# Kernel optimization log

Hardware: AMD Instinct MI355X
Metric: run time of the kernel (lower is better)

Reference implementation:

```python
import jax, jax.numpy as jnp
import numpy as np

N_PROTS = 2048
MOLS_PER_PROT = 8
N_MOLS = N_PROTS * MOLS_PER_PROT
DIM = 768
MARGIN = 0.5


def setup_inputs() -> dict:
    key = jax.random.key(0)
    k1, k2, k3 = jax.random.split(key, 3)
    prot_emb = jax.random.normal(k1, (N_PROTS, DIM), dtype=jnp.float32)
    mol_emb = jax.random.normal(k2, (N_MOLS, DIM), dtype=jnp.float32)
    # L2-normalize like typical CLIP-style retrieval embeddings
    prot_emb = prot_emb / jnp.linalg.norm(prot_emb, axis=1, keepdims=True)
    mol_emb = mol_emb / jnp.linalg.norm(mol_emb, axis=1, keepdims=True)
    # block-structured labels: protein i paired with mols [8i, 8i+8)
    rows = jnp.repeat(jnp.arange(N_PROTS), MOLS_PER_PROT)
    cols = jnp.arange(N_MOLS)
    labels = jnp.zeros((N_PROTS, N_MOLS), dtype=jnp.float32).at[rows, cols].set(1.0)
    # pIC50 values in [2, 10]
    pic50_matrix = 2.0 + 8.0 * jax.random.uniform(k3, (N_PROTS, N_MOLS), dtype=jnp.float32)
    logit_scale = jnp.float32(1.0 / 0.07)
    return {"prot_emb": prot_emb, "mol_emb": mol_emb, "labels": labels,
            "pic50_matrix": pic50_matrix, "logit_scale": logit_scale}


def reference(prot_emb, mol_emb, labels, pic50_matrix, logit_scale):
    n_prots = prot_emb.shape[0]
    n_mols = mol_emb.shape[0]
    sim = jnp.matmul(prot_emb, mol_emb.T) * logit_scale  # [n_prots, n_mols]

    # affinity-weighted InfoNCE (prot -> mol)
    pic50_norm = jnp.clip((pic50_matrix - 2.0) / 8.0, 0.0, 1.0)
    pos_w = labels * pic50_norm
    pos_w = pos_w / (pos_w.sum(axis=1, keepdims=True) + 1e-8)
    loss_p2m = -jnp.sum(pos_w * jax.nn.log_softmax(sim, axis=1)) / n_prots

    # mol -> prot NLL
    mol_labels = jnp.argmax(labels, axis=0)  # [n_mols]
    lsm_m2p = jax.nn.log_softmax(sim.T, axis=1)  # [n_mols, n_prots]
    loss_m2p = -jnp.mean(lsm_m2p[jnp.arange(n_mols), mol_labels])

    # pairwise margin-ranking among positives (exactly MOLS_PER_PROT positives per protein)
    P = MOLS_PER_PROT
    _, pos_idx = jax.lax.top_k(labels, P)  # [n_prots, P] indices of positives
    pos_pic = jnp.take_along_axis(pic50_matrix, pos_idx, axis=1)  # [n_prots, P]
    pos_sc = jnp.take_along_axis(sim, pos_idx, axis=1)            # [n_prots, P]
    dp = pos_pic[:, :, None] - pos_pic[:, None, :]  # [n_prots, P, P]
    ds = pos_sc[:, :, None] - pos_sc[:, None, :]
    pair = jnp.where(dp > 0, jax.nn.relu(MARGIN - ds),
                     jnp.where(dp < 0, jax.nn.relu(MARGIN + ds), 0.0))
    upper = jnp.triu(jnp.ones((P, P), dtype=bool), k=1)  # unordered pairs j<k
    n_pairs = n_prots * (P * (P - 1) // 2)
    ranking_loss = jnp.sum(jnp.where(upper[None], pair, 0.0)) / n_pairs

    # negative push-down
    neg_loss = jnp.mean(jax.nn.relu(sim * (1.0 - labels)))

    total = loss_p2m + loss_m2p + 0.5 * ranking_loss + 0.1 * neg_loss
    return (total, loss_p2m, loss_m2p, ranking_loss, neg_loss)
```

## Files before the change

### kernel.cpp

```cpp
#include <hip/hip_runtime.h>
#include <hip/hip_bf16.h>
#include <math.h>

#define N_PROTS 2048
#define N_MOLS  16384
#define DIM     768
#define SHIFT   16.0f
#define MARGIN  0.5f

typedef __attribute__((ext_vector_type(8))) short short8;
typedef __attribute__((ext_vector_type(4))) float f32x4;
typedef __attribute__((ext_vector_type(4))) unsigned short us4;
typedef __attribute__((ext_vector_type(8))) unsigned short us8;

__device__ __forceinline__ unsigned short bf16rnd(float x) {
    unsigned int u = __float_as_uint(x);
    u += 0x7fffu + ((u >> 16) & 1u);
    return (unsigned short)(u >> 16);
}

__device__ __forceinline__ void gload16(const void* g, void* l) {
    __builtin_amdgcn_global_load_lds(
        (const __attribute__((address_space(1))) unsigned int*)g,
        (__attribute__((address_space(3))) unsigned int*)l, 16, 0, 0);
}

#define ACC_FLOATS 34824
#define PROT_BF_OFF_B 139296ull
#define PROT_BF_BYTES (2048ull*768*2)
#define MOL_BF_OFF_B  (PROT_BF_OFF_B + PROT_BF_BYTES)
#define MOL_BF_BYTES  (16384ull*768*2)
#define WS_NEED       (MOL_BF_OFF_B + MOL_BF_BYTES)

__global__ __launch_bounds__(256)
void convert_bf16(const float* __restrict__ prot, const float* __restrict__ mol,
                  unsigned short* __restrict__ protBf, unsigned short* __restrict__ molBf)
{
    const size_t PROT_G = (size_t)N_PROTS * DIM / 8;
    size_t t = (size_t)blockIdx.x * 256 + threadIdx.x;
    const float* src;
    unsigned short* dst;
    if (t < PROT_G) { src = prot + t * 8; dst = protBf + t * 8; }
    else            { size_t u = t - PROT_G; src = mol + u * 8; dst = molBf + u * 8; }
    float4 v0 = ((const float4*)src)[0];
    float4 v1 = ((const float4*)src)[1];
    us8 o;
    o[0] = bf16rnd(v0.x); o[1] = bf16rnd(v0.y); o[2] = bf16rnd(v0.z); o[3] = bf16rnd(v0.w);
    o[4] = bf16rnd(v1.x); o[5] = bf16rnd(v1.y); o[6] = bf16rnd(v1.z); o[7] = bf16rnd(v1.w);
    *(us8*)dst = o;
}

__global__ __launch_bounds__(256, 3)
void sim_pass_bf16(const unsigned short* __restrict__ protBf,
                   const unsigned short* __restrict__ molBf,
                   const float* __restrict__ scale_p,
                   float* __restrict__ row_se, float* __restrict__ col_se,
                   float* __restrict__ pos_sim, float* __restrict__ scalars)
{
    __shared__ unsigned short As[128][64];
    __shared__ unsigned short Bs[128][64];
    __shared__ float redBuf[4];

    const int tid = threadIdx.x;
    const int l    = blockIdx.x;
    const int xcd  = l & 7;
    const int slot = l >> 3;
    const int bx   = xcd * 16 + (slot & 15);
    const int by   = slot >> 4;
    const int rowBase = by * 128;
    const int colBase = bx * 128;

    const int wave = tid >> 6;
    const int lane = tid & 63;
    const int wr = (wave >> 1) * 64;
    const int wc = (wave & 1) * 64;
    const int l15 = lane & 15;
    const int q   = lane >> 4;

    f32x4 acc[4][4];
#pragma unroll
    for (int i = 0; i < 4; ++i)
#pragma unroll
        for (int j = 0; j < 4; ++j) acc[i][j] = (f32x4){0.f, 0.f, 0.f, 0.f};

    const int rsub = lane >> 3;
    const int cs   = lane & 7;
    const int csrc = (cs ^ rsub) << 3;
    const unsigned short* aP =
        protBf + (size_t)(rowBase + wave * 32 + rsub) * DIM + csrc;
    const unsigned short* bP =
        molBf  + (size_t)(colBase + wave * 32 + rsub) * DIM + csrc;
    unsigned short* ldsA = &As[0][0] + (wave * 32) * 64;
    unsigned short* ldsB = &Bs[0][0] + (wave * 32) * 64;

#pragma unroll 1
    for (int s = 0; s < DIM / 64; ++s) {
        __syncthreads();
#pragma unroll
        for (int i = 0; i < 4; ++i) {
            gload16(aP + (size_t)i * 8 * DIM + s * 64, ldsA + i * 8 * 64);
            gload16(bP + (size_t)i * 8 * DIM + s * 64, ldsB + i * 8 * 64);
        }
        __syncthreads();

#pragma unroll
        for (int kk = 0; kk < 2; ++kk) {
            short8 aF[4], bF[4];
#pragma unroll
            for (int mi = 0; mi < 4; ++mi) {
                const int R = wr + mi * 16 + l15;
                aF[mi] = *(const short8*)&As[R][((kk * 4 + q) ^ (l15 & 7)) << 3];
            }
#pragma unroll
            for (int ni = 0; ni < 4; ++ni) {
                const int R = wc + ni * 16 + l15;
                bF[ni] = *(const short8*)&Bs[R][((kk * 4 + q) ^ (l15 & 7)) << 3];
            }
#pragma unroll
            for (int mi = 0; mi < 4; ++mi)
#pragma unroll
                for (int ni = 0; ni < 4; ++ni)
                    acc[mi][ni] = __builtin_amdgcn_mfma_f32_16x16x32_bf16(
                        aF[mi], bF[ni], acc[mi][ni], 0, 0, 0);
        }
    }

    const float scale = scale_p[0];
    float rsum[4][4];
    float csum[4] = {0.f, 0.f, 0.f, 0.f};
    float rl = 0.f;
#pragma unroll
    for (int mi = 0; mi < 4; ++mi)
#pragma unroll
        for (int r = 0; r < 4; ++r) rsum[mi][r] = 0.f;

#pragma unroll
    for (int mi = 0; mi < 4; ++mi) {
#pragma unroll
        for (int ni = 0; ni < 4; ++ni) {
#pragma unroll
            for (int r = 0; r < 4; ++r) {
                float sim = acc[mi][ni][r] * scale;
                float e = __expf(sim - SHIFT);
                rsum[mi][r] += e;
                csum[ni] += e;
                rl += fmaxf(sim, 0.f);
                int rg = rowBase + wr + mi * 16 + q * 4 + r;
                int cg = colBase + wc + ni * 16 + l15;
                if ((cg >> 3) == rg) pos_sim[cg] = sim;
            }
        }
    }

#pragma unroll
    for (int mi = 0; mi < 4; ++mi) {
#pragma unroll
        for (int r = 0; r < 4; ++r) {
            float v = rsum[mi][r];
            v += __shfl_xor(v, 1); v += __shfl_xor(v, 2);
            v += __shfl_xor(v, 4); v += __shfl_xor(v, 8);
            if (l15 == 0)
                atomicAdd(&row_se[rowBase + wr + mi * 16 + q * 4 + r], v);
        }
    }
#pragma unroll
    for (int ni = 0; ni < 4; ++ni) {
        float v = csum[ni];
        v += __shfl_xor(v, 16); v += __shfl_xor(v, 32);
        if (q == 0)
            atomicAdd(&col_se[colBase + wc + ni * 16 + l15], v);
    }
#pragma unroll
    for (int m = 1; m < 64; m <<= 1) rl += __shfl_xor(rl, m);
    if (lane == 0) redBuf[wave] = rl;
    __syncthreads();
    if (tid == 0)
        atomicAdd(&scalars[0], redBuf[0] + redBuf[1] + redBuf[2] + redBuf[3]);
}

__global__ __launch_bounds__(256, 2)
void sim_pass(const float* __restrict__ prot, const float* __restrict__ mol,
              const float* __restrict__ scale_p,
              float* __restrict__ row_se, float* __restrict__ col_se,
              float* __restrict__ pos_sim, float* __restrict__ scalars)
{
    __shared__ unsigned short As[128][32];
    __shared__ unsigned short Bs[128][32];
    __shared__ float redBuf[4];

    const int tid = threadIdx.x;
    const int rowBase = blockIdx.y * 128;
    const int colBase = blockIdx.x * 128;
    const int wave = tid >> 6;
    const int lane = tid & 63;
    const int wr = (wave >> 1) * 64;
    const int wc = (wave & 1) * 64;
    const int l15 = lane & 15;
    const int q   = lane >> 4;

    f32x4 acc[4][4];
#pragma unroll
    for (int i = 0; i < 4; ++i)
#pragma unroll
        for (int j = 0; j < 4; ++j) acc[i][j] = (f32x4){0.f, 0.f, 0.f, 0.f};

    const float* aBase = prot + (size_t)rowBase * DIM;
    const float* bBase = mol  + (size_t)colBase * DIM;
    float4 aReg[4], bReg[4];
#pragma unroll
    for (int i = 0; i < 4; ++i) {
        int f = tid + 256 * i;
        int row = f >> 3, c4 = f & 7;
        aReg[i] = *(const float4*)(aBase + (size_t)row * DIM + (c4 << 2));
        bReg[i] = *(const float4*)(bBase + (size_t)row * DIM + (c4 << 2));
    }
#pragma unroll 1
    for (int s = 0; s < DIM / 32; ++s) {
#pragma unroll
        for (int i = 0; i < 4; ++i) {
            int f = tid + 256 * i;
            int row = f >> 3, c4 = f & 7;
            us4 av, bv;
            av.x = bf16rnd(aReg[i].x); av.y = bf16rnd(aReg[i].y);
            av.z = bf16rnd(aReg[i].z); av.w = bf16rnd(aReg[i].w);
            bv.x = bf16rnd(bReg[i].x); bv.y = bf16rnd(bReg[i].y);
            bv.z = bf16rnd(bReg[i].z); bv.w = bf16rnd(bReg[i].w);
            *(us4*)&As[row][c4 << 2] = av;
            *(us4*)&Bs[row][c4 << 2] = bv;
        }
        __syncthreads();
        if (s + 1 < DIM / 32) {
            int k0 = (s + 1) * 32;
#pragma unroll
            for (int i = 0; i < 4; ++i) {
                int f = tid + 256 * i;
                int row = f >> 3, c4 = f & 7;
                aReg[i] = *(const float4*)(aBase + (size_t)row * DIM + k0 + (c4 << 2));
                bReg[i] = *(const float4*)(bBase + (size_t)row * DIM + k0 + (c4 << 2));
            }
        }
        short8 aF[4], bF[4];
#pragma unroll
        for (int mi = 0; mi < 4; ++mi) aF[mi] = *(const short8*)&As[wr + mi * 16 + l15][q * 8];
#pragma unroll
        for (int ni = 0; ni < 4; ++ni) bF[ni] = *(const short8*)&Bs[wc + ni * 16 + l15][q * 8];
#pragma unroll
        for (int mi = 0; mi < 4; ++mi)
#pragma unroll
            for (int ni = 0; ni < 4; ++ni)
                acc[mi][ni] = __builtin_amdgcn_mfma_f32_16x16x32_bf16(aF[mi], bF[ni], acc[mi][ni], 0, 0, 0);
        __syncthreads();
    }

    const float scale = scale_p[0];
    float rsum[4][4];
    float csum[4] = {0.f, 0.f, 0.f, 0.f};
    float rl = 0.f;
#pragma unroll
    for (int mi = 0; mi < 4; ++mi)
#pragma unroll
        for (int r = 0; r < 4; ++r) rsum[mi][r] = 0.f;
#pragma unroll
    for (int mi = 0; mi < 4; ++mi) {
#pragma unroll
        for (int ni = 0; ni < 4; ++ni) {
#pragma unroll
            for (int r = 0; r < 4; ++r) {
                float sim = acc[mi][ni][r] * scale;
                float e = __expf(sim - SHIFT);
                rsum[mi][r] += e;
                csum[ni] += e;
                rl += fmaxf(sim, 0.f);
                int rg = rowBase + wr + mi * 16 + q * 4 + r;
                int cg = colBase + wc + ni * 16 + l15;
                if ((cg >> 3) == rg) pos_sim[cg] = sim;
            }
        }
    }
#pragma unroll
    for (int mi = 0; mi < 4; ++mi) {
#pragma unroll
        for (int r = 0; r < 4; ++r) {
            float v = rsum[mi][r];
            v += __shfl_xor(v, 1); v += __shfl_xor(v, 2);
            v += __shfl_xor(v, 4); v += __shfl_xor(v, 8);
            if (l15 == 0)
                atomicAdd(&row_se[rowBase + wr + mi * 16 + q * 4 + r], v);
        }
    }
#pragma unroll
    for (int ni = 0; ni < 4; ++ni) {
        float v = csum[ni];
        v += __shfl_xor(v, 16); v += __shfl_xor(v, 32);
        if (q == 0)
            atomicAdd(&col_se[colBase + wc + ni * 16 + l15], v);
    }
#pragma unroll
    for (int m = 1; m < 64; m <<= 1) rl += __shfl_xor(rl, m);
    if (lane == 0) redBuf[wave] = rl;
    __syncthreads();
    if (tid == 0)
        atomicAdd(&scalars[0], redBuf[0] + redBuf[1] + redBuf[2] + redBuf[3]);
}

__global__ __launch_bounds__(256)
void finalize1(const float* __restrict__ row_se, const float* __restrict__ col_se,
               const float* __restrict__ pos_sim, const float* __restrict__ pic50,
               float* __restrict__ scalars)
{
    int j = blockIdx.x * 256 + threadIdx.x;
    float m2p = SHIFT + __logf(col_se[j]) - pos_sim[j];

    float p2m = 0.f, rank = 0.f, prelu = 0.f;
    if ((j & 7) == 0) {
        int i = j >> 3;
        float s[8], pc[8], pr[8];
#pragma unroll
        for (int p = 0; p < 8; ++p) {
            s[p]  = pos_sim[j + p];
            pr[p] = pic50[(size_t)i * N_MOLS + j + p];
            float x = (pr[p] - 2.0f) * 0.125f;
            pc[p] = fminf(fmaxf(x, 0.f), 1.f);
            prelu += fmaxf(s[p], 0.f);
        }
        float wsum = 1e-8f;
#pragma unroll
        for (int p = 0; p < 8; ++p) wsum += pc[p];
        float lse = SHIFT + __logf(row_se[i]);
        float accp = 0.f;
#pragma unroll
        for (int p = 0; p < 8; ++p) accp += pc[p] * (lse - s[p]);
        p2m = accp / wsum;
#pragma unroll
        for (int a = 0; a < 8; ++a)
#pragma unroll
            for (int b = a + 1; b < 8; ++b) {
                float dp = pr[a] - pr[b];
                float ds = s[a] - s[b];
                float v = (dp > 0.f) ? fmaxf(MARGIN - ds, 0.f)
                        : ((dp < 0.f) ? fmaxf(MARGIN + ds, 0.f) : 0.f);
                rank += v;
            }
    }

#pragma unroll
    for (int m = 1; m < 64; m <<= 1) {
        m2p   += __shfl_xor(m2p, m);
        p2m   += __shfl_xor(p2m, m);
        rank  += __shfl_xor(rank, m);
        prelu += __shfl_xor(prelu, m);
    }
    __shared__ float rbuf[4][4];
    int wave = threadIdx.x >> 6, lane = threadIdx.x & 63;
    if (lane == 0) { rbuf[wave][0] = m2p; rbuf[wave][1] = p2m; rbuf[wave][2] = rank; rbuf[wave][3] = prelu; }
    __syncthreads();
    if (threadIdx.x == 0) {
        float a = 0, b = 0, c = 0, d = 0;
        for (int w = 0; w < 4; ++w) { a += rbuf[w][0]; b += rbuf[w][1]; c += rbuf[w][2]; d += rbuf[w][3]; }
        atomicAdd(&scalars[2], a);
        atomicAdd(&scalars[1], b);
        atomicAdd(&scalars[3], c);
        atomicAdd(&scalars[4], d);
    }
}

__global__ void finalize2(const float* __restrict__ scalars, float* __restrict__ out)
{
    float relu_neg = scalars[0] - scalars[4];
    float p2m  = scalars[1] / (float)N_PROTS;
    float m2p  = scalars[2] / (float)N_MOLS;
    float rank = scalars[3] / ((float)N_PROTS * 28.0f);
    float neg  = relu_neg / ((float)N_PROTS * (float)N_MOLS);
    out[0] = p2m + m2p + 0.5f * rank + 0.1f * neg;
    out[1] = p2m;
    out[2] = m2p;
    out[3] = rank;
    out[4] = neg;
}

extern "C" void kernel_launch(void* const* d_in, const int* in_sizes, int n_in,
                              void* d_out, int out_size, void* d_ws, size_t ws_size,
                              hipStream_t stream) {
    const float* prot   = (const float*)d_in[0];
    const float* mol    = (const float*)d_in[1];
    const float* pic50  = (const float*)d_in[3];
    const float* lscale = (const float*)d_in[4];

    float* ws      = (float*)d_ws;
    float* row_se  = ws;
    float* col_se  = ws + 2048;
    float* pos_sim = ws + 2048 + 16384;
    float* scalars = ws + 2048 + 16384 + 16384;

    hipMemsetAsync(d_ws, 0, (size_t)ACC_FLOATS * sizeof(float), stream);

    if (ws_size >= WS_NEED) {
        unsigned short* protBf = (unsigned short*)((char*)d_ws + PROT_BF_OFF_B);
        unsigned short* molBf  = (unsigned short*)((char*)d_ws + MOL_BF_OFF_B);
        size_t groups = ((size_t)N_PROTS + N_MOLS) * DIM / 8;
        convert_bf16<<<(unsigned)(groups / 256), 256, 0, stream>>>(prot, mol, protBf, molBf);
        sim_pass_bf16<<<2048, 256, 0, stream>>>(protBf, molBf, lscale, row_se, col_se, pos_sim, scalars);
    } else {
        dim3 grid(N_MOLS / 128, N_PROTS / 128);
        sim_pass<<<grid, 256, 0, stream>>>(prot, mol, lscale, row_se, col_se, pos_sim, scalars);
    }
    finalize1<<<N_MOLS / 256, 256, 0, stream>>>(row_se, col_se, pos_sim, pic50, scalars);
    finalize2<<<1, 1, 0, stream>>>(scalars, (float*)d_out);
}
```

Before: 386.3 us.

## Use 256x256 tiles with 4-stage async LDS pipeline in bf16 sim kernel

Replaces the 128x128, 256-thread bf16 GEMM tile with a 256x256 tile on 512 threads (8 waves, each computing 128x64). Global-to-LDS loads go through a 4-slot ring buffer with three tiles prefetched ahead, a vmcnt wait plus a single barrier per k-step, and prefetches interleaved between MFMA groups under raised wave priority. The aim is more reuse per loaded byte and loads that overlap the MFMA work instead of being serialized behind two barriers. The cost is more registers (128 accumulators per lane), fewer blocks (512), and a ring that relies on a hand-tuned vmcnt count, plus dummy reloads in the tail that refetch already-used k-tiles.

```diff
diff --git a/kernel.cpp b/kernel.cpp
--- a/kernel.cpp
+++ b/kernel.cpp
@@ -50,117 +50,132 @@
     *(us8*)dst = o;
 }
 
-__global__ __launch_bounds__(256, 3)
-void sim_pass_bf16(const unsigned short* __restrict__ protBf,
-                   const unsigned short* __restrict__ molBf,
-                   const float* __restrict__ scale_p,
-                   float* __restrict__ row_se, float* __restrict__ col_se,
-                   float* __restrict__ pos_sim, float* __restrict__ scalars)
+__global__ __launch_bounds__(512, 2)
+void sim_pass_bf16_v2(const unsigned short* __restrict__ protBf,
+                      const unsigned short* __restrict__ molBf,
+                      const float* __restrict__ scale_p,
+                      float* __restrict__ row_se, float* __restrict__ col_se,
+                      float* __restrict__ pos_sim, float* __restrict__ scalars)
 {
-    __shared__ unsigned short As[128][64];
-    __shared__ unsigned short Bs[128][64];
-    __shared__ float redBuf[4];
+    __shared__ unsigned short As[4][256][32];
+    __shared__ unsigned short Bs[4][256][32];
+    __shared__ float redBuf[8];
 
     const int tid = threadIdx.x;
-    const int l    = blockIdx.x;
-    const int xcd  = l & 7;
-    const int slot = l >> 3;
-    const int bx   = xcd * 16 + (slot & 15);
-    const int by   = slot >> 4;
-    const int rowBase = by * 128;
-    const int colBase = bx * 128;
+    const int bid  = blockIdx.x;
+    const int xcd  = bid & 7;
+    const int sl8  = bid >> 3;
+    const int bx   = xcd * 8 + (sl8 & 7);
+    const int by   = sl8 >> 3;
+    const int rowBase = by * 256;
+    const int colBase = bx * 256;
 
     const int wave = tid >> 6;
     const int lane = tid & 63;
-    const int wr = (wave >> 1) * 64;
-    const int wc = (wave & 1) * 64;
+    const int wm = wave >> 2;
+    const int wn = wave & 3;
     const int l15 = lane & 15;
     const int q   = lane >> 4;
 
-    f32x4 acc[4][4];
-#pragma unroll
-    for (int i = 0; i < 4; ++i)
+    const int rsub = lane >> 2;
+    const int cs   = lane & 3;
+    const int swz  = (cs ^ (rsub & 3)) << 3;
+    const unsigned short* aP =
+        protBf + (size_t)(rowBase + wave * 32 + rsub) * DIM + swz;
+    const unsigned short* bP =
+        molBf  + (size_t)(colBase + wave * 32 + rsub) * DIM + swz;
+
+#define STAGE_A(sl, kt) do { \
+    gload16(aP + (size_t)(kt) * 32,                    &As[sl][wave * 32][0]);      \
+    gload16(aP + (size_t)(kt) * 32 + (size_t)16 * DIM, &As[sl][wave * 32 + 16][0]); \
+} while (0)
+#define STAGE_B(sl, kt) do { \
+    gload16(bP + (size_t)(kt) * 32,                    &Bs[sl][wave * 32][0]);      \
+    gload16(bP + (size_t)(kt) * 32 + (size_t)16 * DIM, &Bs[sl][wave * 32 + 16][0]); \
+} while (0)
+
+    f32x4 acc[8][4];
+#pragma unroll
+    for (int i = 0; i < 8; ++i)
 #pragma unroll
         for (int j = 0; j < 4; ++j) acc[i][j] = (f32x4){0.f, 0.f, 0.f, 0.f};
 
-    const int rsub = lane >> 3;
-    const int cs   = lane & 7;
-    const int csrc = (cs ^ rsub) << 3;
-    const unsigned short* aP =
-        protBf + (size_t)(rowBase + wave * 32 + rsub) * DIM + csrc;
-    const unsigned short* bP =
-        molBf  + (size_t)(colBase + wave * 32 + rsub) * DIM + csrc;
-    unsigned short* ldsA = &As[0][0] + (wave * 32) * 64;
-    unsigned short* ldsB = &Bs[0][0] + (wave * 32) * 64;
+    STAGE_A(0, 0); STAGE_B(0, 0);
+    STAGE_A(1, 1); STAGE_B(1, 1);
+    STAGE_A(2, 2); STAGE_B(2, 2);
+
+    const int fArow = wm * 128 + l15;
+    const int fBrow = wn * 64 + l15;
+    const int fsw   = (q ^ (l15 & 3)) << 3;
 
 #pragma unroll 1
-    for (int s = 0; s < DIM / 64; ++s) {
-        __syncthreads();
-#pragma unroll
-        for (int i = 0; i < 4; ++i) {
-            gload16(aP + (size_t)i * 8 * DIM + s * 64, ldsA + i * 8 * 64);
-            gload16(bP + (size_t)i * 8 * DIM + s * 64, ldsB + i * 8 * 64);
-        }
-        __syncthreads();
-
-#pragma unroll
-        for (int kk = 0; kk < 2; ++kk) {
-            short8 aF[4], bF[4];
-#pragma unroll
-            for (int mi = 0; mi < 4; ++mi) {
-                const int R = wr + mi * 16 + l15;
-                aF[mi] = *(const short8*)&As[R][((kk * 4 + q) ^ (l15 & 7)) << 3];
-            }
-#pragma unroll
-            for (int ni = 0; ni < 4; ++ni) {
-                const int R = wc + ni * 16 + l15;
-                bF[ni] = *(const short8*)&Bs[R][((kk * 4 + q) ^ (l15 & 7)) << 3];
-            }
-#pragma unroll
-            for (int mi = 0; mi < 4; ++mi)
-#pragma unroll
-                for (int ni = 0; ni < 4; ++ni)
-                    acc[mi][ni] = __builtin_amdgcn_mfma_f32_16x16x32_bf16(
-                        aF[mi], bF[ni], acc[mi][ni], 0, 0, 0);
-        }
-    }
+    for (int t = 0; t < 24; ++t) {
+        const int sl   = t & 3;
+        const int pf   = (t + 3) & 3;
+        const int kpre = (t < 21) ? (t + 3) : (t - 5);
+        asm volatile("s_waitcnt vmcnt(8)" ::: "memory");
+        __builtin_amdgcn_s_barrier();
+
+        short8 aF[4], bF[4];
+#pragma unroll
+        for (int ni = 0; ni < 4; ++ni)
+            bF[ni] = *(const short8*)&Bs[sl][fBrow + ni * 16][fsw];
+#pragma unroll
+        for (int mi = 0; mi < 4; ++mi)
+            aF[mi] = *(const short8*)&As[sl][fArow + mi * 16][fsw];
+        STAGE_A(pf, kpre);
+        __builtin_amdgcn_s_setprio(1);
+#pragma unroll
+        for (int mi = 0; mi < 4; ++mi)
+#pragma unroll
+            for (int ni = 0; ni < 4; ++ni)
+                acc[mi][ni] = __builtin_amdgcn_mfma_f32_16x16x32_bf16(
+                    aF[mi], bF[ni], acc[mi][ni], 0, 0, 0);
+        __builtin_amdgcn_s_setprio(0);
+
+#pragma unroll
+        for (int mi = 0; mi < 4; ++mi)
+            aF[mi] = *(const short8*)&As[sl][fArow + 64 + mi * 16][fsw];
+        STAGE_B(pf, kpre);
+        __builtin_amdgcn_s_setprio(1);
+#pragma unroll
+        for (int mi = 0; mi < 4; ++mi)
+#pragma unroll
+            for (int ni = 0; ni < 4; ++ni)
+                acc[4 + mi][ni] = __builtin_amdgcn_mfma_f32_16x16x32_bf16(
+                    aF[mi], bF[ni], acc[4 + mi][ni], 0, 0, 0);
+        __builtin_amdgcn_s_setprio(0);
+    }
+#undef STAGE_A
+#undef STAGE_B
 
     const float scale = scale_p[0];
-    float rsum[4][4];
     float csum[4] = {0.f, 0.f, 0.f, 0.f};
     float rl = 0.f;
 #pragma unroll
-    for (int mi = 0; mi < 4; ++mi)
-#pragma unroll
-        for (int r = 0; r < 4; ++r) rsum[mi][r] = 0.f;
-
-#pragma unroll
-    for (int mi = 0; mi < 4; ++mi) {
+    for (int mi = 0; mi < 8; ++mi) {
+        float rs[4] = {0.f, 0.f, 0.f, 0.f};
 #pragma unroll
         for (int ni = 0; ni < 4; ++ni) {
 #pragma unroll
             for (int r = 0; r < 4; ++r) {
                 float sim = acc[mi][ni][r] * scale;
                 float e = __expf(sim - SHIFT);
-                rsum[mi][r] += e;
+                rs[r] += e;
                 csum[ni] += e;
                 rl += fmaxf(sim, 0.f);
-                int rg = rowBase + wr + mi * 16 + q * 4 + r;
-                int cg = colBase + wc + ni * 16 + l15;
+                int rg = rowBase + wm * 128 + mi * 16 + q * 4 + r;
+                int cg = colBase + wn * 64 + ni * 16 + l15;
                 if ((cg >> 3) == rg) pos_sim[cg] = sim;
             }
         }
-    }
-
-#pragma unroll
-    for (int mi = 0; mi < 4; ++mi) {
 #pragma unroll
         for (int r = 0; r < 4; ++r) {
-            float v = rsum[mi][r];
+            float v = rs[r];
             v += __shfl_xor(v, 1); v += __shfl_xor(v, 2);
             v += __shfl_xor(v, 4); v += __shfl_xor(v, 8);
             if (l15 == 0)
-                atomicAdd(&row_se[rowBase + wr + mi * 16 + q * 4 + r], v);
+                atomicAdd(&row_se[rowBase + wm * 128 + mi * 16 + q * 4 + r], v);
         }
     }
 #pragma unroll
@@ -168,14 +183,18 @@
         float v = csum[ni];
         v += __shfl_xor(v, 16); v += __shfl_xor(v, 32);
         if (q == 0)
-            atomicAdd(&col_se[colBase + wc + ni * 16 + l15], v);
+            atomicAdd(&col_se[colBase + wn * 64 + ni * 16 + l15], v);
     }
 #pragma unroll
     for (int m = 1; m < 64; m <<= 1) rl += __shfl_xor(rl, m);
     if (lane == 0) redBuf[wave] = rl;
     __syncthreads();
-    if (tid == 0)
-        atomicAdd(&scalars[0], redBuf[0] + redBuf[1] + redBuf[2] + redBuf[3]);
+    if (tid == 0) {
+        float s = 0.f;
+#pragma unroll
+        for (int w = 0; w < 8; ++w) s += redBuf[w];
+        atomicAdd(&scalars[0], s);
+    }
 }
 
 __global__ __launch_bounds__(256, 2)
@@ -399,7 +418,7 @@
         unsigned short* molBf  = (unsigned short*)((char*)d_ws + MOL_BF_OFF_B);
         size_t groups = ((size_t)N_PROTS + N_MOLS) * DIM / 8;
         convert_bf16<<<(unsigned)(groups / 256), 256, 0, stream>>>(prot, mol, protBf, molBf);
-        sim_pass_bf16<<<2048, 256, 0, stream>>>(protBf, molBf, lscale, row_se, col_se, pos_sim, scalars);
+        sim_pass_bf16_v2<<<512, 512, 0, stream>>>(protBf, molBf, lscale, row_se, col_se, pos_sim, scalars);
     } else {
         dim3 grid(N_MOLS / 128, N_PROTS / 128);
         sim_pass<<<grid, 256, 0, stream>>>(prot, mol, lscale, row_se, col_se, pos_sim, scalars);
```

New measurement: 381.1 us. About the same (-1.3%).
